# Kernel tuning notes

Hardware: AMD Instinct MI355X
Metric: run time of the kernel (lower is better)

The kernel has to match this reference:

```python
import jax, jax.numpy as jnp
import numpy as np


def setup_inputs() -> dict:
    key = jax.random.key(0)
    k1, k2, k3 = jax.random.split(key, 3)
    B, S, Q, K, D = 64, 512, 800, 4, 64
    q_data = jax.random.normal(k1, (B, S, Q), dtype=jnp.float32)
    r_data = jax.random.randint(k2, (B, S), 0, K)
    # learned params (xavier-ish scale)
    Wq = jax.random.normal(k3, (D, Q), dtype=jnp.float32) * (0.5 * (2.0 / (Q + D)) ** 0.5)
    bq = jnp.zeros((D,), dtype=jnp.float32)
    Wr = jax.random.normal(jax.random.fold_in(key, 7), (1, K), dtype=jnp.float32) * (0.5 * (2.0 / (K + 1)) ** 0.5)
    br = jnp.zeros((1,), dtype=jnp.float32)
    return {"q_data": q_data, "r_data": r_data, "Wq": Wq, "bq": bq,
            "Wr": Wr, "br": br, "n_questions": Q, "n_cats": K}


def reference(q_data, r_data, Wq, bq, Wr, br, n_questions, n_cats):
    # Vectorized over (batch, seq): original looped over t in python.
    K = n_cats
    k_idx = jnp.arange(K, dtype=q_data.dtype)                      # [K]
    dist = jnp.abs(k_idx[None, None, :] - r_data[..., None].astype(q_data.dtype)) / (K - 1)  # [B,S,K]
    weights = jnp.maximum(1.0 - dist, 0.0)                        # [B,S,K]
    # response_weights: Linear(K -> 1) then sigmoid -> scalar gate per (b,s)
    gate = jax.nn.sigmoid(jnp.einsum('bsk,ok->bso', weights, Wr) + br)  # [B,S,1]
    weighted_q = q_data * gate                                    # [B,S,Q]
    # question_embed: Linear(Q -> D)
    out = jnp.einsum('bsq,dq->bsd', weighted_q, Wq) + bq          # [B,S,D]
    return out
```

## Files before the change

### kernel.cpp

```cpp
#include <hip/hip_runtime.h>
#include <hip/hip_bf16.h>


#define QD 800
#define DD 64
#define M_TOTAL 32768
#define KT 25
#define DEPTH 5

typedef __attribute__((ext_vector_type(8))) short bf16x8;
typedef __attribute__((ext_vector_type(4))) float f32x4;

static __device__ __forceinline__ short f2bf(float f) {
  union { __hip_bfloat16 h; short s; } u;
  u.h = __float2bfloat16(f);
  return u.s;
}

static __device__ __forceinline__ bf16x8 pack8(f32x4 lo, f32x4 hi) {
  bf16x8 r;
  r[0] = f2bf(lo.x); r[1] = f2bf(lo.y); r[2] = f2bf(lo.z); r[3] = f2bf(lo.w);
  r[4] = f2bf(hi.x); r[5] = f2bf(hi.y); r[6] = f2bf(hi.z); r[7] = f2bf(hi.w);
  return r;
}

static __device__ __forceinline__ bf16x8 load_split8(const float* __restrict__ p) {
  return pack8(*reinterpret_cast<const f32x4*>(p),
               *reinterpret_cast<const f32x4*>(p + 16));
}

__global__ void convert_wq_kernel(const float* __restrict__ Wq, short* __restrict__ Bb) {
  int idx = blockIdx.x * 256 + threadIdx.x;
  int kt = idx >> 8;
  int acc = (idx >> 6) & 3;
  int lane = idx & 63;
  int l15 = lane & 15, lhi = lane >> 4;
  const float* p = Wq + (acc * 16 + l15) * QD + kt * 32 + lhi * 4;
  *reinterpret_cast<bf16x8*>(Bb + (size_t)idx * 8) = load_split8(p);
}

__global__ __launch_bounds__(256, 2) void sold_kernel(
    const float* __restrict__ q, const int* __restrict__ rdat,
    const short* __restrict__ Bb, const float* __restrict__ bq,
    const float* __restrict__ Wr, const float* __restrict__ br,
    float* __restrict__ out) {
  const int lane = threadIdx.x & 63;
  const int wave = threadIdx.x >> 6;
  const int l15 = lane & 15;
  const int lhi = lane >> 4;
  const int m0 = blockIdx.x * 64 + wave * 16;

  const float* ap = q + (size_t)(m0 + l15) * QD + lhi * 4;
  const short* bp = Bb + (size_t)lane * 8;

  f32x4 aLo[DEPTH], aHi[DEPTH];
  bf16x8 bfr[DEPTH][4];

#pragma unroll
  for (int s = 0; s < DEPTH; ++s) {
    const float* a = ap + s * 32;
    aLo[s] = *reinterpret_cast<const f32x4*>(a);
    aHi[s] = *reinterpret_cast<const f32x4*>(a + 16);
    const short* p = bp + s * 2048;
    bfr[s][0] = *reinterpret_cast<const bf16x8*>(p + 0 * 512);
    bfr[s][1] = *reinterpret_cast<const bf16x8*>(p + 1 * 512);
    bfr[s][2] = *reinterpret_cast<const bf16x8*>(p + 2 * 512);
    bfr[s][3] = *reinterpret_cast<const bf16x8*>(p + 3 * 512);
  }

  f32x4 acc0 = {0.f, 0.f, 0.f, 0.f};
  f32x4 acc1 = {0.f, 0.f, 0.f, 0.f};
  f32x4 acc2 = {0.f, 0.f, 0.f, 0.f};
  f32x4 acc3 = {0.f, 0.f, 0.f, 0.f};

#pragma unroll
  for (int kt = 0; kt < KT; ++kt) {
    const int s = kt % DEPTH;
    bf16x8 a = pack8(aLo[s], aHi[s]);
    acc0 = __builtin_amdgcn_mfma_f32_16x16x32_bf16(a, bfr[s][0], acc0, 0, 0, 0);
    acc1 = __builtin_amdgcn_mfma_f32_16x16x32_bf16(a, bfr[s][1], acc1, 0, 0, 0);
    acc2 = __builtin_amdgcn_mfma_f32_16x16x32_bf16(a, bfr[s][2], acc2, 0, 0, 0);
    acc3 = __builtin_amdgcn_mfma_f32_16x16x32_bf16(a, bfr[s][3], acc3, 0, 0, 0);
    const int nx = kt + DEPTH;
    if (nx < KT) {
      const float* a2 = ap + nx * 32;
      aLo[s] = *reinterpret_cast<const f32x4*>(a2);
      aHi[s] = *reinterpret_cast<const f32x4*>(a2 + 16);
      const short* p = bp + nx * 2048;
      bfr[s][0] = *reinterpret_cast<const bf16x8*>(p + 0 * 512);
      bfr[s][1] = *reinterpret_cast<const bf16x8*>(p + 1 * 512);
      bfr[s][2] = *reinterpret_cast<const bf16x8*>(p + 2 * 512);
      bfr[s][3] = *reinterpret_cast<const bf16x8*>(p + 3 * 512);
    }
    __builtin_amdgcn_sched_barrier(0);
  }

  float wr[4] = {Wr[0], Wr[1], Wr[2], Wr[3]};
  float brv = br[0];
  float lut[4];
  const float inv3 = 1.0f / 3.0f;
#pragma unroll
  for (int r = 0; r < 4; ++r) {
    float s = brv;
#pragma unroll
    for (int k = 0; k < 4; ++k) {
      float w = fmaxf(1.0f - fabsf((float)(k - r)) * inv3, 0.0f);
      s += w * wr[k];
    }
    lut[r] = 1.0f / (1.0f + __expf(-s));
  }

  float bqv0 = bq[0 * 16 + l15];
  float bqv1 = bq[1 * 16 + l15];
  float bqv2 = bq[2 * 16 + l15];
  float bqv3 = bq[3 * 16 + l15];

#pragma unroll
  for (int r = 0; r < 4; ++r) {
    int row = m0 + lhi * 4 + r;
    float g = lut[rdat[row]];
    float* orow = out + (size_t)row * DD + l15;
    orow[0]  = acc0[r] * g + bqv0;
    orow[16] = acc1[r] * g + bqv1;
    orow[32] = acc2[r] * g + bqv2;
    orow[48] = acc3[r] * g + bqv3;
  }
}

__global__ __launch_bounds__(256, 2) void sold_direct(
    const float* __restrict__ q, const int* __restrict__ rdat,
    const float* __restrict__ Wq, const float* __restrict__ bq,
    const float* __restrict__ Wr, const float* __restrict__ br,
    float* __restrict__ out) {
  const int lane = threadIdx.x & 63;
  const int wave = threadIdx.x >> 6;
  const int l15 = lane & 15;
  const int lhi = lane >> 4;
  const int m0 = blockIdx.x * 64 + wave * 16;
  const float* aptr = q + (size_t)(m0 + l15) * QD + lhi * 4;
  const float* w0 = Wq + (0 * 16 + l15) * QD + lhi * 4;
  const float* w1 = Wq + (1 * 16 + l15) * QD + lhi * 4;
  const float* w2 = Wq + (2 * 16 + l15) * QD + lhi * 4;
  const float* w3 = Wq + (3 * 16 + l15) * QD + lhi * 4;
  f32x4 acc0 = {0.f,0.f,0.f,0.f}, acc1 = {0.f,0.f,0.f,0.f};
  f32x4 acc2 = {0.f,0.f,0.f,0.f}, acc3 = {0.f,0.f,0.f,0.f};
#pragma unroll 5
  for (int kt = 0; kt < KT; ++kt) {
    bf16x8 a  = load_split8(aptr + kt * 32);
    bf16x8 b0 = load_split8(w0 + kt * 32);
    bf16x8 b1 = load_split8(w1 + kt * 32);
    bf16x8 b2 = load_split8(w2 + kt * 32);
    bf16x8 b3 = load_split8(w3 + kt * 32);
    acc0 = __builtin_amdgcn_mfma_f32_16x16x32_bf16(a, b0, acc0, 0, 0, 0);
    acc1 = __builtin_amdgcn_mfma_f32_16x16x32_bf16(a, b1, acc1, 0, 0, 0);
    acc2 = __builtin_amdgcn_mfma_f32_16x16x32_bf16(a, b2, acc2, 0, 0, 0);
    acc3 = __builtin_amdgcn_mfma_f32_16x16x32_bf16(a, b3, acc3, 0, 0, 0);
  }
  float wr[4] = {Wr[0], Wr[1], Wr[2], Wr[3]};
  float brv = br[0], lut[4];
  const float inv3 = 1.0f / 3.0f;
#pragma unroll
  for (int r = 0; r < 4; ++r) {
    float s = brv;
#pragma unroll
    for (int k = 0; k < 4; ++k)
      s += fmaxf(1.0f - fabsf((float)(k - r)) * inv3, 0.0f) * wr[k];
    lut[r] = 1.0f / (1.0f + __expf(-s));
  }
  float bqv0 = bq[l15], bqv1 = bq[16 + l15], bqv2 = bq[32 + l15], bqv3 = bq[48 + l15];
#pragma unroll
  for (int r = 0; r < 4; ++r) {
    int row = m0 + lhi * 4 + r;
    float g = lut[rdat[row]];
    float* orow = out + (size_t)row * DD + l15;
    orow[0]  = acc0[r] * g + bqv0;
    orow[16] = acc1[r] * g + bqv1;
    orow[32] = acc2[r] * g + bqv2;
    orow[48] = acc3[r] * g + bqv3;
  }
}

extern "C" void kernel_launch(void* const* d_in, const int* in_sizes, int n_in,
                              void* d_out, int out_size, void* d_ws, size_t ws_size,
                              hipStream_t stream) {
  const float* q    = (const float*)d_in[0];
  const int*   rdat = (const int*)d_in[1];
  const float* Wq   = (const float*)d_in[2];
  const float* bq   = (const float*)d_in[3];
  const float* Wr   = (const float*)d_in[4];
  const float* br   = (const float*)d_in[5];
  float* out = (float*)d_out;

  const size_t need_ws = (size_t)KT * 2048 * sizeof(short);
  if (ws_size >= need_ws) {
    short* Bb = (short*)d_ws;
    convert_wq_kernel<<<KT, 256, 0, stream>>>(Wq, Bb);
    sold_kernel<<<M_TOTAL / 64, 256, 0, stream>>>(q, rdat, Bb, bq, Wr, br, out);
  } else {
    sold_direct<<<M_TOTAL / 64, 256, 0, stream>>>(q, rdat, Wq, bq, Wr, br, out);
  }
}
```

Measured before the change: 170.3 us.

## Split K across wave pairs with LDS reduction and raise occupancy

Each block now covers 32 rows instead of 64. Its four waves form two row panels times two K halves. Wq is padded to 26 K-tiles with a zero tile so each half runs 13 MFMA steps, and the upper-half waves pass their partial accumulators to the lower-half waves through shared memory. Prefetch depth drops from 5 to 3 and the launch bound asks for 4 blocks per SM, both to free registers. The goal is more memory requests in flight for this latency-bound streaming GEMM, at the cost of a __syncthreads, an LDS round trip and one redundant padded K-step.

```diff
diff --git a/kernel.cpp b/kernel.cpp
--- a/kernel.cpp
+++ b/kernel.cpp
@@ -6,7 +6,9 @@
 #define DD 64
 #define M_TOTAL 32768
 #define KT 25
-#define DEPTH 5
+#define KT_PAD 26
+#define HALF_KT 13
+#define DEPTH 3
 
 typedef __attribute__((ext_vector_type(8))) short bf16x8;
 typedef __attribute__((ext_vector_type(4))) float f32x4;
@@ -35,23 +37,32 @@
   int acc = (idx >> 6) & 3;
   int lane = idx & 63;
   int l15 = lane & 15, lhi = lane >> 4;
+  if (kt == KT) {
+    bf16x8 z = {};
+    *reinterpret_cast<bf16x8*>(Bb + (size_t)idx * 8) = z;
+    return;
+  }
   const float* p = Wq + (acc * 16 + l15) * QD + kt * 32 + lhi * 4;
   *reinterpret_cast<bf16x8*>(Bb + (size_t)idx * 8) = load_split8(p);
 }
 
-__global__ __launch_bounds__(256, 2) void sold_kernel(
+__global__ __launch_bounds__(256, 4) void sold_split(
     const float* __restrict__ q, const int* __restrict__ rdat,
     const short* __restrict__ Bb, const float* __restrict__ bq,
     const float* __restrict__ Wr, const float* __restrict__ br,
     float* __restrict__ out) {
   const int lane = threadIdx.x & 63;
   const int wave = threadIdx.x >> 6;
+  const int panel = wave >> 1;
+  const int khalf = wave & 1;
   const int l15 = lane & 15;
   const int lhi = lane >> 4;
-  const int m0 = blockIdx.x * 64 + wave * 16;
-
-  const float* ap = q + (size_t)(m0 + l15) * QD + lhi * 4;
-  const short* bp = Bb + (size_t)lane * 8;
+  const int m0 = blockIdx.x * 32 + panel * 16;
+
+  __shared__ float red[2][16][64];
+
+  const float* ap = q + (size_t)(m0 + l15) * QD + lhi * 4 + khalf * (HALF_KT * 32);
+  const short* bp = Bb + (size_t)lane * 8 + (size_t)khalf * (HALF_KT * 2048);
 
   f32x4 aLo[DEPTH], aHi[DEPTH];
   bf16x8 bfr[DEPTH][4];
@@ -74,16 +85,17 @@
   f32x4 acc3 = {0.f, 0.f, 0.f, 0.f};
 
 #pragma unroll
-  for (int kt = 0; kt < KT; ++kt) {
-    const int s = kt % DEPTH;
+  for (int j = 0; j < HALF_KT; ++j) {
+    const int s = j % DEPTH;
     bf16x8 a = pack8(aLo[s], aHi[s]);
     acc0 = __builtin_amdgcn_mfma_f32_16x16x32_bf16(a, bfr[s][0], acc0, 0, 0, 0);
     acc1 = __builtin_amdgcn_mfma_f32_16x16x32_bf16(a, bfr[s][1], acc1, 0, 0, 0);
     acc2 = __builtin_amdgcn_mfma_f32_16x16x32_bf16(a, bfr[s][2], acc2, 0, 0, 0);
     acc3 = __builtin_amdgcn_mfma_f32_16x16x32_bf16(a, bfr[s][3], acc3, 0, 0, 0);
-    const int nx = kt + DEPTH;
-    if (nx < KT) {
-      const float* a2 = ap + nx * 32;
+    const int nx = j + DEPTH;
+    if (nx < HALF_KT) {
+      const int aoff = (nx == HALF_KT - 1) ? (khalf ? 352 : 384) : nx * 32;
+      const float* a2 = ap + aoff;
       aLo[s] = *reinterpret_cast<const f32x4*>(a2);
       aHi[s] = *reinterpret_cast<const f32x4*>(a2 + 16);
       const short* p = bp + nx * 2048;
@@ -93,6 +105,26 @@
       bfr[s][3] = *reinterpret_cast<const bf16x8*>(p + 3 * 512);
     }
     __builtin_amdgcn_sched_barrier(0);
+  }
+
+  if (khalf) {
+#pragma unroll
+    for (int r = 0; r < 4; ++r) {
+      red[panel][0  + r][lane] = acc0[r];
+      red[panel][4  + r][lane] = acc1[r];
+      red[panel][8  + r][lane] = acc2[r];
+      red[panel][12 + r][lane] = acc3[r];
+    }
+  }
+  __syncthreads();
+  if (khalf) return;
+
+#pragma unroll
+  for (int r = 0; r < 4; ++r) {
+    acc0[r] += red[panel][0  + r][lane];
+    acc1[r] += red[panel][4  + r][lane];
+    acc2[r] += red[panel][8  + r][lane];
+    acc3[r] += red[panel][12 + r][lane];
   }
 
   float wr[4] = {Wr[0], Wr[1], Wr[2], Wr[3]};
@@ -191,11 +223,11 @@
   const float* br   = (const float*)d_in[5];
   float* out = (float*)d_out;
 
-  const size_t need_ws = (size_t)KT * 2048 * sizeof(short);
+  const size_t need_ws = (size_t)KT_PAD * 2048 * sizeof(short);
   if (ws_size >= need_ws) {
     short* Bb = (short*)d_ws;
-    convert_wq_kernel<<<KT, 256, 0, stream>>>(Wq, Bb);
-    sold_kernel<<<M_TOTAL / 64, 256, 0, stream>>>(q, rdat, Bb, bq, Wr, br, out);
+    convert_wq_kernel<<<KT_PAD, 256, 0, stream>>>(Wq, Bb);
+    sold_split<<<M_TOTAL / 32, 256, 0, stream>>>(q, rdat, Bb, bq, Wr, br, out);
   } else {
     sold_direct<<<M_TOTAL / 64, 256, 0, stream>>>(q, rdat, Wq, bq, Wr, br, out);
   }
```

New measurement: 172.1 us. Within noise of the previous version (+1.1%).
